# Kernel tuning notes

Hardware: AMD Instinct MI355X
Metric: run time of the kernel (lower is better)

## Reference

```python
import jax, jax.numpy as jnp
import numpy as np

AVG_NODES = 50.0  # matches init avg_nodes
EPS = 1e-9


def setup_inputs() -> dict:
    key = jax.random.key(0)
    k1, k2, k3 = jax.random.split(key, 3)
    N, D, G, OUT = 500000, 128, 10000, 128
    x = jax.random.normal(k1, (N, D), dtype=jnp.float32)
    batch = jnp.sort(jax.random.randint(k2, (N,), 0, G)).astype(jnp.int64)
    W = (jax.random.normal(k3, (5 * D, OUT), dtype=jnp.float32) / np.float32(np.sqrt(5 * D)))
    b = jnp.zeros((OUT,), dtype=jnp.float32)
    return {"x": x, "batch": batch, "W": W, "b": b, "num_segments": G}


def reference(x, batch, W, b, num_segments):
    G = num_segments  # static Python int
    N = x.shape[0]
    ones = jnp.ones((N,), dtype=x.dtype)
    counts = jnp.maximum(jax.ops.segment_sum(ones, batch, G), 1.0)[:, None]  # [G,1]
    x_sum = jax.ops.segment_sum(x, batch, G)            # [G,D]
    x_mean = x_sum / counts
    x_min = jax.ops.segment_min(x, batch, G)
    x_max = jax.ops.segment_max(x, batch, G)
    mean_sq = jax.ops.segment_sum(x * x, batch, G) / counts
    std = jnp.sqrt(jnp.maximum(mean_sq - x_mean ** 2, EPS))
    feats = jnp.concatenate(
        [x_sum * (1.0 / jnp.sqrt(jnp.float32(AVG_NODES))), x_mean, x_min, x_max, std],
        axis=1,
    )  # [G, 5D]
    return feats @ W + b
```

## Files before the change

### kernel.cpp

```cpp
#include <hip/hip_runtime.h>
#include <float.h>
#include <math.h>

#define D 128
#define FIVE_D 640
#define NOUT 128
#define GR 8

__global__ void seg_offsets_kernel(const int* __restrict__ batch, int* __restrict__ offs,
                                   int N, int G) {
    int g = blockIdx.x * blockDim.x + threadIdx.x;
    if (g > G) return;
    if (g == G) { offs[G] = N; return; }
    int lo = 0, hi = N;
    while (lo < hi) {
        int mid = (lo + hi) >> 1;
        if (batch[mid] < g) lo = mid + 1; else hi = mid;
    }
    offs[g] = lo;
}

__global__ __launch_bounds__(64) void seg_stats_kernel(const float* __restrict__ x,
                                                       const int* __restrict__ offs,
                                                       float* __restrict__ feats) {
    const int g = blockIdx.x;
    const int lane = threadIdx.x;
    const int half = lane >> 5;
    const int c = lane & 31;
    const int start = offs[g];
    const int end   = offs[g + 1];

    float4 s  = make_float4(0.f, 0.f, 0.f, 0.f);
    float4 q  = make_float4(0.f, 0.f, 0.f, 0.f);
    float4 mn = make_float4(FLT_MAX, FLT_MAX, FLT_MAX, FLT_MAX);
    float4 mx = make_float4(-FLT_MAX, -FLT_MAX, -FLT_MAX, -FLT_MAX);

    const float4* xp = reinterpret_cast<const float4*>(x) + c;

    auto acc = [&](float4 v) {
        s.x += v.x; s.y += v.y; s.z += v.z; s.w += v.w;
        q.x = fmaf(v.x, v.x, q.x); q.y = fmaf(v.y, v.y, q.y);
        q.z = fmaf(v.z, v.z, q.z); q.w = fmaf(v.w, v.w, q.w);
        mn.x = fminf(mn.x, v.x); mn.y = fminf(mn.y, v.y);
        mn.z = fminf(mn.z, v.z); mn.w = fminf(mn.w, v.w);
        mx.x = fmaxf(mx.x, v.x); mx.y = fmaxf(mx.y, v.y);
        mx.z = fmaxf(mx.z, v.z); mx.w = fmaxf(mx.w, v.w);
    };

    int base = start;
    for (; base + 8 <= end; base += 8) {
        float4 v0 = xp[(size_t)(base + 0 + half) * 32];
        float4 v1 = xp[(size_t)(base + 2 + half) * 32];
        float4 v2 = xp[(size_t)(base + 4 + half) * 32];
        float4 v3 = xp[(size_t)(base + 6 + half) * 32];
        acc(v0); acc(v1); acc(v2); acc(v3);
    }
    for (; base + 2 <= end; base += 2) {
        float4 v = xp[(size_t)(base + half) * 32];
        acc(v);
    }
    if (base < end && half == 0) {
        float4 v = xp[(size_t)base * 32];
        acc(v);
    }

    s.x += __shfl_xor(s.x, 32); s.y += __shfl_xor(s.y, 32);
    s.z += __shfl_xor(s.z, 32); s.w += __shfl_xor(s.w, 32);
    q.x += __shfl_xor(q.x, 32); q.y += __shfl_xor(q.y, 32);
    q.z += __shfl_xor(q.z, 32); q.w += __shfl_xor(q.w, 32);
    mn.x = fminf(mn.x, __shfl_xor(mn.x, 32)); mn.y = fminf(mn.y, __shfl_xor(mn.y, 32));
    mn.z = fminf(mn.z, __shfl_xor(mn.z, 32)); mn.w = fminf(mn.w, __shfl_xor(mn.w, 32));
    mx.x = fmaxf(mx.x, __shfl_xor(mx.x, 32)); mx.y = fmaxf(mx.y, __shfl_xor(mx.y, 32));
    mx.z = fmaxf(mx.z, __shfl_xor(mx.z, 32)); mx.w = fmaxf(mx.w, __shfl_xor(mx.w, 32));

    if (half == 0) {
        const float cnt = (float)max(end - start, 1);
        const float inv = 1.0f / cnt;
        const float SC = 0.14142135623730950488f;
        float4 mean = make_float4(s.x * inv, s.y * inv, s.z * inv, s.w * inv);
        float4 sd;
        sd.x = sqrtf(fmaxf(q.x * inv - mean.x * mean.x, 1e-9f));
        sd.y = sqrtf(fmaxf(q.y * inv - mean.y * mean.y, 1e-9f));
        sd.z = sqrtf(fmaxf(q.z * inv - mean.z * mean.z, 1e-9f));
        sd.w = sqrtf(fmaxf(q.w * inv - mean.w * mean.w, 1e-9f));
        float4 ssc = make_float4(s.x * SC, s.y * SC, s.z * SC, s.w * SC);

        float* f = feats + (size_t)g * FIVE_D + 4 * c;
        *reinterpret_cast<float4*>(f)         = ssc;
        *reinterpret_cast<float4*>(f + D)     = mean;
        *reinterpret_cast<float4*>(f + 2 * D) = mn;
        *reinterpret_cast<float4*>(f + 3 * D) = mx;
        *reinterpret_cast<float4*>(f + 4 * D) = sd;
    }
}

__global__ __launch_bounds__(256) void gemm_kernel(const float* __restrict__ feats,
                                                   const float* __restrict__ W,
                                                   const float* __restrict__ b,
                                                   float* __restrict__ out, int G) {
    __shared__ float lf[GR * FIVE_D];
    const int tid = threadIdx.x;
    const int lane = tid & 63;
    const int wave = tid >> 6;
    const int g0 = blockIdx.x * GR;

    {
        const float4* src = reinterpret_cast<const float4*>(feats + (size_t)g0 * FIVE_D);
        float4* dst = reinterpret_cast<float4*>(lf);
        #pragma unroll
        for (int i = 0; i < (GR * FIVE_D) / 4 / 256; ++i)
            dst[i * 256 + tid] = src[i * 256 + tid];
    }
    __syncthreads();

    const int r0 = wave * 2, r1 = wave * 2 + 1;
    float a00 = 0.f, a01 = 0.f, a10 = 0.f, a11 = 0.f;

    for (int k = 0; k < FIVE_D; k += 4) {
        const float w00 = W[(k + 0) * NOUT + lane];
        const float w01 = W[(k + 0) * NOUT + 64 + lane];
        const float w10 = W[(k + 1) * NOUT + lane];
        const float w11 = W[(k + 1) * NOUT + 64 + lane];
        const float w20 = W[(k + 2) * NOUT + lane];
        const float w21 = W[(k + 2) * NOUT + 64 + lane];
        const float w30 = W[(k + 3) * NOUT + lane];
        const float w31 = W[(k + 3) * NOUT + 64 + lane];
        const float4 f0 = *reinterpret_cast<const float4*>(&lf[r0 * FIVE_D + k]);
        const float4 f1 = *reinterpret_cast<const float4*>(&lf[r1 * FIVE_D + k]);
        a00 = fmaf(f0.x, w00, a00); a01 = fmaf(f0.x, w01, a01);
        a10 = fmaf(f1.x, w00, a10); a11 = fmaf(f1.x, w01, a11);
        a00 = fmaf(f0.y, w10, a00); a01 = fmaf(f0.y, w11, a01);
        a10 = fmaf(f1.y, w10, a10); a11 = fmaf(f1.y, w11, a11);
        a00 = fmaf(f0.z, w20, a00); a01 = fmaf(f0.z, w21, a01);
        a10 = fmaf(f1.z, w20, a10); a11 = fmaf(f1.z, w21, a11);
        a00 = fmaf(f0.w, w30, a00); a01 = fmaf(f0.w, w31, a01);
        a10 = fmaf(f1.w, w30, a10); a11 = fmaf(f1.w, w31, a11);
    }

    const float b0 = b[lane];
    const float b1 = b[64 + lane];
    if (g0 + r0 < G) {
        out[(size_t)(g0 + r0) * NOUT + lane]      = a00 + b0;
        out[(size_t)(g0 + r0) * NOUT + 64 + lane] = a01 + b1;
    }
    if (g0 + r1 < G) {
        out[(size_t)(g0 + r1) * NOUT + lane]      = a10 + b0;
        out[(size_t)(g0 + r1) * NOUT + 64 + lane] = a11 + b1;
    }
}

extern "C" void kernel_launch(void* const* d_in, const int* in_sizes, int n_in,
                              void* d_out, int out_size, void* d_ws, size_t ws_size,
                              hipStream_t stream) {
    const float* x     = (const float*)d_in[0];
    const int*   batch = (const int*)d_in[1];
    const float* W     = (const float*)d_in[2];
    const float* b     = (const float*)d_in[3];
    float* out = (float*)d_out;

    const int N = in_sizes[0] / D;
    const int G = out_size / NOUT;

    int*   offs  = (int*)d_ws;
    float* feats = (float*)((char*)d_ws + 65536);

    seg_offsets_kernel<<<(G + 1 + 255) / 256, 256, 0, stream>>>(batch, offs, N, G);
    seg_stats_kernel<<<G, 64, 0, stream>>>(x, offs, feats);
    gemm_kernel<<<(G + GR - 1) / GR, 256, 0, stream>>>(feats, W, b, out, G);
}
```

Before: 425.5 us.

## Use one-wave GEMM blocks computing eight rows with register double-buffering

Replaces the 256-thread GEMM that staged features in shared memory with a 64-thread kernel where each wave computes eight output rows. Each W element loaded is reused across eight rows instead of two, reducing repeated W reads from cache, and loads of the next k-chunk are double-buffered in registers ahead of the FMAs. Feature rows are read directly from global memory as broadcast loads. Fewer, smaller blocks reduce occupancy and may expose latency.

New measurement: 478.2 us. +12.4%, slower.

```diff
diff --git a/kernel.cpp b/kernel.cpp
--- a/kernel.cpp
+++ b/kernel.cpp
@@ -5,7 +5,7 @@
 #define D 128
 #define FIVE_D 640
 #define NOUT 128
-#define GR 8
+#define GW 8
 
 __global__ void seg_offsets_kernel(const int* __restrict__ batch, int* __restrict__ offs,
                                    int N, int G) {
@@ -94,58 +94,72 @@
     }
 }
 
-__global__ __launch_bounds__(256) void gemm_kernel(const float* __restrict__ feats,
-                                                   const float* __restrict__ W,
-                                                   const float* __restrict__ b,
-                                                   float* __restrict__ out, int G) {
-    __shared__ float lf[GR * FIVE_D];
-    const int tid = threadIdx.x;
-    const int lane = tid & 63;
-    const int wave = tid >> 6;
-    const int g0 = blockIdx.x * GR;
+#define LOADK(SUF, kk) do {                                                              \
+    const int k_ = (kk);                                                                 \
+    _Pragma("unroll")                                                                    \
+    for (int r = 0; r < GW; ++r)                                                         \
+        f##SUF[r] = *reinterpret_cast<const float4*>(fr[r] + k_);                        \
+    _Pragma("unroll")                                                                    \
+    for (int j = 0; j < 4; ++j) {                                                        \
+        w##SUF##0[j] = Wp0[(size_t)(k_ + j) * NOUT];                                     \
+        w##SUF##1[j] = Wp1[(size_t)(k_ + j) * NOUT];                                     \
+    }                                                                                    \
+} while (0)
 
-    {
-        const float4* src = reinterpret_cast<const float4*>(feats + (size_t)g0 * FIVE_D);
-        float4* dst = reinterpret_cast<float4*>(lf);
-        #pragma unroll
-        for (int i = 0; i < (GR * FIVE_D) / 4 / 256; ++i)
-            dst[i * 256 + tid] = src[i * 256 + tid];
-    }
-    __syncthreads();
+#define FMAK(SUF) do {                                                                   \
+    _Pragma("unroll")                                                                    \
+    for (int r = 0; r < GW; ++r) {                                                       \
+        a0[r] = fmaf(f##SUF[r].x, w##SUF##0[0], a0[r]);                                  \
+        a1[r] = fmaf(f##SUF[r].x, w##SUF##1[0], a1[r]);                                  \
+        a0[r] = fmaf(f##SUF[r].y, w##SUF##0[1], a0[r]);                                  \
+        a1[r] = fmaf(f##SUF[r].y, w##SUF##1[1], a1[r]);                                  \
+        a0[r] = fmaf(f##SUF[r].z, w##SUF##0[2], a0[r]);                                  \
+        a1[r] = fmaf(f##SUF[r].z, w##SUF##1[2], a1[r]);                                  \
+        a0[r] = fmaf(f##SUF[r].w, w##SUF##0[3], a0[r]);                                  \
+        a1[r] = fmaf(f##SUF[r].w, w##SUF##1[3], a1[r]);                                  \
+    }                                                                                    \
+} while (0)
 
-    const int r0 = wave * 2, r1 = wave * 2 + 1;
-    float a00 = 0.f, a01 = 0.f, a10 = 0.f, a11 = 0.f;
+__global__ __launch_bounds__(64) void gemm_kernel(const float* __restrict__ feats,
+                                                  const float* __restrict__ W,
+                                                  const float* __restrict__ b,
+                                                  float* __restrict__ out, int G) {
+    const int lane = threadIdx.x;
+    const int g0 = blockIdx.x * GW;
+    if (g0 >= G) return;
 
-    for (int k = 0; k < FIVE_D; k += 4) {
-        const float w00 = W[(k + 0) * NOUT + lane];
-        const float w01 = W[(k + 0) * NOUT + 64 + lane];
-        const float w10 = W[(k + 1) * NOUT + lane];
-        const float w11 = W[(k + 1) * NOUT + 64 + lane];
-        const float w20 = W[(k + 2) * NOUT + lane];
-        const float w21 = W[(k + 2) * NOUT + 64 + lane];
-        const float w30 = W[(k + 3) * NOUT + lane];
-        const float w31 = W[(k + 3) * NOUT + 64 + lane];
-        const float4 f0 = *reinterpret_cast<const float4*>(&lf[r0 * FIVE_D + k]);
-        const float4 f1 = *reinterpret_cast<const float4*>(&lf[r1 * FIVE_D + k]);
-        a00 = fmaf(f0.x, w00, a00); a01 = fmaf(f0.x, w01, a01);
-        a10 = fmaf(f1.x, w00, a10); a11 = fmaf(f1.x, w01, a11);
-        a00 = fmaf(f0.y, w10, a00); a01 = fmaf(f0.y, w11, a01);
-        a10 = fmaf(f1.y, w10, a10); a11 = fmaf(f1.y, w11, a11);
-        a00 = fmaf(f0.z, w20, a00); a01 = fmaf(f0.z, w21, a01);
-        a10 = fmaf(f1.z, w20, a10); a11 = fmaf(f1.z, w21, a11);
-        a00 = fmaf(f0.w, w30, a00); a01 = fmaf(f0.w, w31, a01);
-        a10 = fmaf(f1.w, w30, a10); a11 = fmaf(f1.w, w31, a11);
+    const float* fr[GW];
+    #pragma unroll
+    for (int r = 0; r < GW; ++r)
+        fr[r] = feats + (size_t)min(g0 + r, G - 1) * FIVE_D;
+
+    const float* Wp0 = W + lane;
+    const float* Wp1 = W + 64 + lane;
+
+    float a0[GW], a1[GW];
+    #pragma unroll
+    for (int r = 0; r < GW; ++r) { a0[r] = 0.f; a1[r] = 0.f; }
+
+    float4 fA[GW], fB[GW];
+    float wA0[4], wA1[4], wB0[4], wB1[4];
+
+    LOADK(A, 0);
+    for (int k = 0; k < FIVE_D; k += 8) {
+        LOADK(B, k + 4);
+        FMAK(A);
+        if (k + 8 < FIVE_D) LOADK(A, k + 8);
+        FMAK(B);
     }
 
     const float b0 = b[lane];
     const float b1 = b[64 + lane];
-    if (g0 + r0 < G) {
-        out[(size_t)(g0 + r0) * NOUT + lane]      = a00 + b0;
-        out[(size_t)(g0 + r0) * NOUT + 64 + lane] = a01 + b1;
-    }
-    if (g0 + r1 < G) {
-        out[(size_t)(g0 + r1) * NOUT + lane]      = a10 + b0;
-        out[(size_t)(g0 + r1) * NOUT + 64 + lane] = a11 + b1;
+    #pragma unroll
+    for (int r = 0; r < GW; ++r) {
+        const int g = g0 + r;
+        if (g < G) {
+            out[(size_t)g * NOUT + lane]      = a0[r] + b0;
+            out[(size_t)g * NOUT + 64 + lane] = a1[r] + b1;
+        }
     }
 }
 
@@ -166,5 +180,5 @@
 
     seg_offsets_kernel<<<(G + 1 + 255) / 256, 256, 0, stream>>>(batch, offs, N, G);
     seg_stats_kernel<<<G, 64, 0, stream>>>(x, offs, feats);
-    gemm_kernel<<<(G + GR - 1) / GR, 256, 0, stream>>>(feats, W, b, out, G);
+    gemm_kernel<<<(G + GW - 1) / GW, 64, 0, stream>>>(feats, W, b, out, G);
 }
```
